# Kernel optimization log

Measured on AMD Instinct MI355X. Metric: run time of the kernel, lower is better.

Reference implementation:

```python
import jax, jax.numpy as jnp
import numpy as np

N = 16384       # input points
D_IN = 64       # feature dim
D_OUT = 128     # output dim
STRIDE = 4      # downsampling stride -> M = N // STRIDE sampled points
NSAMPLE = 16    # hard-coded in __init__
BN_EPS = 1e-5


def setup_inputs() -> dict:
    key = jax.random.key(0)
    k1, k2, k3 = jax.random.split(key, 3)
    p = jax.random.normal(k1, (N, 3), jnp.float32)
    x = jax.random.normal(k2, (N, D_IN), jnp.float32)
    o = jnp.array([N], jnp.int32)  # single-cloud offsets
    # mlp params: Linear(d_in+3, d_out) + BatchNorm1d(d_out)
    W = jax.random.normal(k3, (D_IN + 3, D_OUT), jnp.float32) * 0.05
    b = jnp.zeros((D_OUT,), jnp.float32)
    gamma = jnp.ones((D_OUT,), jnp.float32)
    beta = jnp.zeros((D_OUT,), jnp.float32)
    return {"p": p, "x": x, "o": o, "W": W, "b": b, "gamma": gamma, "beta": beta}


def fps(p, m):
    """Furthest point sampling: returns m indices into p [N,3]. Sequential by nature."""
    n = p.shape[0]
    dists = jnp.full((n,), jnp.inf, p.dtype)
    idxs = jnp.zeros((m,), jnp.int32)  # start from point 0 (pointops convention)

    def body(i, carry):
        idxs, dists = carry
        last = p[idxs[i - 1]]                      # [3]
        d = jnp.sum((p - last) ** 2, axis=1)       # [N]
        dists = jnp.minimum(dists, d)
        return idxs.at[i].set(jnp.argmax(dists).astype(jnp.int32)), dists

    idxs, _ = jax.lax.fori_loop(1, m, body, (idxs, dists))
    return idxs


def reference(p, x, o, W, b, gamma, beta):
    m = p.shape[0] // STRIDE  # static
    # --- furthest point sampling (non-differentiable index op, as in pointops) ---
    s_idx = fps(jax.lax.stop_gradient(p), m)
    n_p = p[s_idx]                                             # [M,3]
    # --- query-and-group: kNN of each sampled point over all N points ---
    d2 = (jnp.sum(n_p ** 2, axis=1)[:, None]
          + jnp.sum(p ** 2, axis=1)[None, :]
          - 2.0 * n_p @ p.T)                                   # [M,N]
    _, nn_idx = jax.lax.top_k(-d2, NSAMPLE)                    # [M,K]
    pj = p[nn_idx] - n_p[:, None, :]                           # [M,K,3] relative coords
    xj = x[nn_idx]                                             # [M,K,D_IN]
    # normalize relative coords by max neighbor norm per sampled point
    nrm = jnp.linalg.norm(pj, axis=-1, keepdims=True)          # [M,K,1]
    pj = pj / (jnp.max(nrm, axis=1, keepdims=True) + 1e-8)
    feat = jnp.concatenate([pj, xj], axis=-1).max(axis=1)      # [M, 3+D_IN] max-pool
    # --- MLP: Linear + BatchNorm1d (training stats) + ReLU ---
    h = feat @ W + b                                           # [M, D_OUT]
    mean = jnp.mean(h, axis=0)
    var = jnp.var(h, axis=0)
    h = (h - mean) / jnp.sqrt(var + BN_EPS) * gamma + beta
    x_out = jax.nn.relu(h)
    n_o = jnp.array([m], jnp.int32)
    return (n_p, x_out, n_o)
```

## Files before the change

### kernel.cpp

```cpp
#include <hip/hip_runtime.h>

#define N_PTS 16384
#define M_PTS 4096
#define D_INF 64
#define D_OUTF 128
#define KNN 16
#define DF 67

__global__ __launch_bounds__(256) void sp_kernel(const float* __restrict__ p,
                                                 float* __restrict__ spn) {
  int j = blockIdx.x * 256 + threadIdx.x;
  float a = p[3 * j], b = p[3 * j + 1], c = p[3 * j + 2];
  spn[j] = __fadd_rn(__fadd_rn(__fmul_rn(a, a), __fmul_rn(b, b)), __fmul_rn(c, c));
}

#define FPS_T 512
#define FPS_PPT 32

__global__ __launch_bounds__(FPS_T) void fps_kernel(const float* __restrict__ p,
                                                    int* __restrict__ sidx,
                                                    float* __restrict__ np_out) {
  const int t = threadIdx.x;
  float px[FPS_PPT], py[FPS_PPT], pz[FPS_PPT], dd[FPS_PPT];
#pragma unroll
  for (int k = 0; k < FPS_PPT; ++k) {
    int j = t + (k << 9);
    px[k] = p[3 * j]; py[k] = p[3 * j + 1]; pz[k] = p[3 * j + 2];
    dd[k] = INFINITY;
  }
  __shared__ float s_wmax[FPS_T / 64];
  __shared__ float s_last[3];
  __shared__ int s_widx;
  if (t == 0) {
    s_widx = 0x7FFFFFFF;
    s_last[0] = px[0]; s_last[1] = py[0]; s_last[2] = pz[0];
    sidx[0] = 0;
    np_out[0] = px[0]; np_out[1] = py[0]; np_out[2] = pz[0];
  }
  __syncthreads();
  for (int i = 1; i < M_PTS; ++i) {
    float lx = s_last[0], ly = s_last[1], lz = s_last[2];
    float tmax = -INFINITY;
#pragma unroll
    for (int k = 0; k < FPS_PPT; ++k) {
      float dx = __fsub_rn(px[k], lx);
      float dy = __fsub_rn(py[k], ly);
      float dz = __fsub_rn(pz[k], lz);
      float d = __fadd_rn(__fadd_rn(__fmul_rn(dx, dx), __fmul_rn(dy, dy)),
                          __fmul_rn(dz, dz));
      float nd = fminf(dd[k], d);
      dd[k] = nd;
      tmax = fmaxf(tmax, nd);
    }
    float wmax = tmax;
#pragma unroll
    for (int off = 32; off >= 1; off >>= 1)
      wmax = fmaxf(wmax, __shfl_xor(wmax, off));
    if ((t & 63) == 0) s_wmax[t >> 6] = wmax;
    __syncthreads();
    float gmax = s_wmax[0];
#pragma unroll
    for (int wv = 1; wv < FPS_T / 64; ++wv) gmax = fmaxf(gmax, s_wmax[wv]);
    int m = 0x7FFFFFFF;
    float cx = 0.f, cy = 0.f, cz = 0.f;
    if (tmax == gmax) {
#pragma unroll
      for (int k = FPS_PPT - 1; k >= 0; --k) {
        if (dd[k] == gmax) { m = t + (k << 9); cx = px[k]; cy = py[k]; cz = pz[k]; }
      }
      atomicMin(&s_widx, m);
    }
    __syncthreads();
    int widx = s_widx;
    if (m != 0x7FFFFFFF && m == widx) {
      s_last[0] = cx; s_last[1] = cy; s_last[2] = cz;
      s_widx = 0x7FFFFFFF;
      sidx[i] = m;
      np_out[3 * i] = cx; np_out[3 * i + 1] = cy; np_out[3 * i + 2] = cz;
    }
    __syncthreads();
  }
}

__global__ __launch_bounds__(256) void knn_feat_kernel(const float* __restrict__ p,
                                                       const float* __restrict__ x,
                                                       const float* __restrict__ spn,
                                                       const int* __restrict__ sidx,
                                                       float* __restrict__ feat) {
  __shared__ float cd[4][256];
  __shared__ int ci[4][256];
  __shared__ int cnt[4];
  __shared__ int s_nn[4][KNN];
  const int w = threadIdx.x >> 6;
  const int lane = threadIdx.x & 63;
  const int q = (blockIdx.x << 2) + w;
  const int qi = sidx[q];
  const float qx = p[3 * qi], qy = p[3 * qi + 1], qz = p[3 * qi + 2];
  const float sn = spn[qi];
  if (lane == 0) cnt[w] = 0;
  float lmin = INFINITY;
  for (int it = 0; it < N_PTS / 64; ++it) {
    int j = lane + (it << 6);
    float dot = __fmaf_rn(qz, p[3 * j + 2],
                 __fmaf_rn(qy, p[3 * j + 1], __fmul_rn(qx, p[3 * j])));
    float d2 = __fsub_rn(__fadd_rn(sn, spn[j]), __fmul_rn(2.0f, dot));
    lmin = fminf(lmin, d2);
  }
  float mv = lmin;
  float tau = INFINITY;
#pragma unroll
  for (int r = 0; r < KNN; ++r) {
    float rmin = mv;
#pragma unroll
    for (int off = 32; off >= 1; off >>= 1) rmin = fminf(rmin, __shfl_xor(rmin, off));
    tau = rmin;
    unsigned long long msk = __ballot(mv == rmin);
    if (lane == (int)(__ffsll(msk) - 1)) mv = INFINITY;
  }
  __syncthreads();
  for (int it = 0; it < N_PTS / 64; ++it) {
    int j = lane + (it << 6);
    float dot = __fmaf_rn(qz, p[3 * j + 2],
                 __fmaf_rn(qy, p[3 * j + 1], __fmul_rn(qx, p[3 * j])));
    float d2 = __fsub_rn(__fadd_rn(sn, spn[j]), __fmul_rn(2.0f, dot));
    if (d2 <= tau) {
      int pos = atomicAdd(&cnt[w], 1);
      if (pos < 256) { cd[w][pos] = d2; ci[w][pos] = j; }
    }
  }
  __syncthreads();
  int C = min(cnt[w], 256);
  float vv[4]; int ii[4];
#pragma unroll
  for (int s = 0; s < 4; ++s) {
    int pos = lane + (s << 6);
    bool ok = pos < C;
    vv[s] = ok ? cd[w][pos] : INFINITY;
    ii[s] = ok ? ci[w][pos] : 0x7FFFFFFF;
  }
#pragma unroll
  for (int r = 0; r < KNN; ++r) {
    float bv = vv[0]; int bi = ii[0]; int bs = 0;
#pragma unroll
    for (int s = 1; s < 4; ++s) {
      bool tk = (vv[s] < bv) || (vv[s] == bv && ii[s] < bi);
      bv = tk ? vv[s] : bv; bi = tk ? ii[s] : bi; bs = tk ? s : bs;
    }
    float rv = bv; int ri = bi;
#pragma unroll
    for (int off = 32; off >= 1; off >>= 1) {
      float ov = __shfl_xor(rv, off); int oi = __shfl_xor(ri, off);
      bool tk = (ov < rv) || (ov == rv && oi < ri);
      rv = tk ? ov : rv; ri = tk ? oi : ri;
    }
    if (bi == ri) {
#pragma unroll
      for (int s = 0; s < 4; ++s) if (s == bs) vv[s] = INFINITY;
    }
    if (lane == 0) s_nn[w][r] = ri;
  }
  __syncthreads();
  float ax = -INFINITY, ay = -INFINITY, az = -INFINITY, nr = -INFINITY;
  if (lane < KNN) {
    int jn = s_nn[w][lane];
    ax = __fsub_rn(p[3 * jn], qx);
    ay = __fsub_rn(p[3 * jn + 1], qy);
    az = __fsub_rn(p[3 * jn + 2], qz);
    nr = sqrtf(__fadd_rn(__fadd_rn(__fmul_rn(ax, ax), __fmul_rn(ay, ay)),
                         __fmul_rn(az, az)));
  }
  float mnr = nr, mx = ax, my = ay, mz = az;
#pragma unroll
  for (int off = 32; off >= 1; off >>= 1) {
    mnr = fmaxf(mnr, __shfl_xor(mnr, off));
    mx = fmaxf(mx, __shfl_xor(mx, off));
    my = fmaxf(my, __shfl_xor(my, off));
    mz = fmaxf(mz, __shfl_xor(mz, off));
  }
  if (lane == 0) {
    float sden = __fadd_rn(mnr, 1e-8f);
    feat[q * DF + 0] = mx / sden;
    feat[q * DF + 1] = my / sden;
    feat[q * DF + 2] = mz / sden;
  }
  float fm = -INFINITY;
#pragma unroll
  for (int k = 0; k < KNN; ++k) {
    int jn = s_nn[w][k];
    fm = fmaxf(fm, x[(jn << 6) + lane]);
  }
  feat[q * DF + 3 + lane] = fm;
}

__global__ __launch_bounds__(128) void mlp_kernel(const float* __restrict__ feat,
                                                  const float* __restrict__ W,
                                                  const float* __restrict__ b,
                                                  float* __restrict__ h) {
  int mrow = blockIdx.x;
  int o = threadIdx.x;
  const float* fr = feat + mrow * DF;
  float acc = b[o];
#pragma unroll
  for (int k = 0; k < DF; ++k) acc = __fmaf_rn(fr[k], W[k * D_OUTF + o], acc);
  h[mrow * D_OUTF + o] = acc;
}

__global__ __launch_bounds__(256) void stats_kernel(const float* __restrict__ h,
                                                    const float* __restrict__ gamma,
                                                    const float* __restrict__ beta,
                                                    float* __restrict__ scsh) {
  int o = blockIdx.x;
  int t = threadIdx.x;
  float s = 0.f, s2 = 0.f;
  for (int mrow = t; mrow < M_PTS; mrow += 256) {
    float v = h[mrow * D_OUTF + o];
    s += v;
    s2 = __fmaf_rn(v, v, s2);
  }
#pragma unroll
  for (int off = 32; off >= 1; off >>= 1) {
    s += __shfl_xor(s, off);
    s2 += __shfl_xor(s2, off);
  }
  __shared__ float as1[4], as2[4];
  if ((t & 63) == 0) { as1[t >> 6] = s; as2[t >> 6] = s2; }
  __syncthreads();
  if (t == 0) {
    float ts = ((as1[0] + as1[1]) + as1[2]) + as1[3];
    float ts2 = ((as2[0] + as2[1]) + as2[2]) + as2[3];
    float mean = ts / (float)M_PTS;
    float var = ts2 / (float)M_PTS - mean * mean;
    var = fmaxf(var, 0.f);
    float sc = gamma[o] / sqrtf(var + 1e-5f);
    scsh[o] = sc;
    scsh[D_OUTF + o] = beta[o] - mean * sc;
  }
}

__global__ __launch_bounds__(256) void bn_kernel(const float* __restrict__ h,
                                                 const float* __restrict__ scsh,
                                                 float* __restrict__ out) {
  int idx = blockIdx.x * 256 + threadIdx.x;
  int o = idx & (D_OUTF - 1);
  float v = __fmaf_rn(h[idx], scsh[o], scsh[D_OUTF + o]);
  out[M_PTS * 3 + idx] = fmaxf(v, 0.f);
  if (idx == 0) out[M_PTS * 3 + M_PTS * D_OUTF] = 4096.0f;
}

extern "C" void kernel_launch(void* const* d_in, const int* in_sizes, int n_in,
                              void* d_out, int out_size, void* d_ws, size_t ws_size,
                              hipStream_t stream) {
  const float* p     = (const float*)d_in[0];
  const float* x     = (const float*)d_in[1];
  const float* W     = (const float*)d_in[3];
  const float* b     = (const float*)d_in[4];
  const float* gamma = (const float*)d_in[5];
  const float* beta  = (const float*)d_in[6];
  float* out = (float*)d_out;

  float* wsf  = (float*)d_ws;
  int*   sidx = (int*)d_ws;
  float* spn  = wsf + 4096;
  float* feat = spn + N_PTS;
  float* h    = feat + M_PTS * DF;
  float* scsh = h + M_PTS * D_OUTF;

  sp_kernel<<<N_PTS / 256, 256, 0, stream>>>(p, spn);
  fps_kernel<<<1, FPS_T, 0, stream>>>(p, sidx, out);
  knn_feat_kernel<<<M_PTS / 4, 256, 0, stream>>>(p, x, spn, sidx, feat);
  mlp_kernel<<<M_PTS, D_OUTF, 0, stream>>>(feat, W, b, h);
  stats_kernel<<<D_OUTF, 256, 0, stream>>>(h, gamma, beta, scsh);
  bn_kernel<<<(M_PTS * D_OUTF) / 256, 256, 0, stream>>>(h, scsh, out);
}
```

Before: 7.321 ms.

## Use argmax shuffle reduction with double-buffered shared slots in FPS

Rewrites the per-iteration FPS reduction to carry (value, index) pairs through the wave shuffle and a double-buffered shared array. This cuts three barriers per iteration down to one and removes the shared atomicMin and the broadcast of the last point. Every thread now reloads the winner's coordinates from global memory (an L1/L2 hit), and the launch bounds hint asks for two blocks per CU, which may constrain register allocation for the 128 per-thread point registers.

```diff
diff --git a/kernel.cpp b/kernel.cpp
--- a/kernel.cpp
+++ b/kernel.cpp
@@ -17,10 +17,12 @@
 #define FPS_T 512
 #define FPS_PPT 32
 
-__global__ __launch_bounds__(FPS_T) void fps_kernel(const float* __restrict__ p,
-                                                    int* __restrict__ sidx,
-                                                    float* __restrict__ np_out) {
+__global__ __launch_bounds__(FPS_T, 2) void fps_kernel(const float* __restrict__ p,
+                                                       int* __restrict__ sidx,
+                                                       float* __restrict__ np_out) {
   const int t = threadIdx.x;
+  const int wave = t >> 6;
+  const int lane = t & 63;
   float px[FPS_PPT], py[FPS_PPT], pz[FPS_PPT], dd[FPS_PPT];
 #pragma unroll
   for (int k = 0; k < FPS_PPT; ++k) {
@@ -28,19 +30,17 @@
     px[k] = p[3 * j]; py[k] = p[3 * j + 1]; pz[k] = p[3 * j + 2];
     dd[k] = INFINITY;
   }
-  __shared__ float s_wmax[FPS_T / 64];
-  __shared__ float s_last[3];
-  __shared__ int s_widx;
+  __shared__ float s_v[2][FPS_T / 64];
+  __shared__ int s_i[2][FPS_T / 64];
+  float lx = p[0], ly = p[1], lz = p[2];
   if (t == 0) {
-    s_widx = 0x7FFFFFFF;
-    s_last[0] = px[0]; s_last[1] = py[0]; s_last[2] = pz[0];
     sidx[0] = 0;
-    np_out[0] = px[0]; np_out[1] = py[0]; np_out[2] = pz[0];
-  }
-  __syncthreads();
+    np_out[0] = lx; np_out[1] = ly; np_out[2] = lz;
+  }
   for (int i = 1; i < M_PTS; ++i) {
-    float lx = s_last[0], ly = s_last[1], lz = s_last[2];
-    float tmax = -INFINITY;
+    const int b = i & 1;
+    float bestv = -INFINITY;
+    int besti = 0x7FFFFFFF;
 #pragma unroll
     for (int k = 0; k < FPS_PPT; ++k) {
       float dx = __fsub_rn(px[k], lx);
@@ -50,35 +50,30 @@
                           __fmul_rn(dz, dz));
       float nd = fminf(dd[k], d);
       dd[k] = nd;
-      tmax = fmaxf(tmax, nd);
-    }
-    float wmax = tmax;
-#pragma unroll
-    for (int off = 32; off >= 1; off >>= 1)
-      wmax = fmaxf(wmax, __shfl_xor(wmax, off));
-    if ((t & 63) == 0) s_wmax[t >> 6] = wmax;
+      if (nd > bestv) besti = t + (k << 9);
+      bestv = fmaxf(bestv, nd);
+    }
+#pragma unroll
+    for (int off = 32; off >= 1; off >>= 1) {
+      float ov = __shfl_xor(bestv, off);
+      int oi = __shfl_xor(besti, off);
+      if (ov > bestv || (ov == bestv && oi < besti)) { bestv = ov; besti = oi; }
+    }
+    if (lane == 0) { s_v[b][wave] = bestv; s_i[b][wave] = besti; }
     __syncthreads();
-    float gmax = s_wmax[0];
-#pragma unroll
-    for (int wv = 1; wv < FPS_T / 64; ++wv) gmax = fmaxf(gmax, s_wmax[wv]);
-    int m = 0x7FFFFFFF;
-    float cx = 0.f, cy = 0.f, cz = 0.f;
-    if (tmax == gmax) {
-#pragma unroll
-      for (int k = FPS_PPT - 1; k >= 0; --k) {
-        if (dd[k] == gmax) { m = t + (k << 9); cx = px[k]; cy = py[k]; cz = pz[k]; }
-      }
-      atomicMin(&s_widx, m);
-    }
-    __syncthreads();
-    int widx = s_widx;
-    if (m != 0x7FFFFFFF && m == widx) {
-      s_last[0] = cx; s_last[1] = cy; s_last[2] = cz;
-      s_widx = 0x7FFFFFFF;
-      sidx[i] = m;
-      np_out[3 * i] = cx; np_out[3 * i + 1] = cy; np_out[3 * i + 2] = cz;
-    }
-    __syncthreads();
+    float gv = s_v[b][0];
+    int gi = s_i[b][0];
+#pragma unroll
+    for (int w = 1; w < FPS_T / 64; ++w) {
+      float vw = s_v[b][w];
+      int iw = s_i[b][w];
+      if (vw > gv || (vw == gv && iw < gi)) { gv = vw; gi = iw; }
+    }
+    lx = p[3 * gi]; ly = p[3 * gi + 1]; lz = p[3 * gi + 2];
+    if (t == 0) {
+      sidx[i] = gi;
+      np_out[3 * i] = lx; np_out[3 * i + 1] = ly; np_out[3 * i + 2] = lz;
+    }
   }
 }
 
```

Result: slower. 9.374 ms (+28.1%).
